# Kernel tuning notes

Hardware: AMD Instinct MI355X
Metric: run time of the kernel (lower is better)

## Reference

```python
import jax, jax.numpy as jnp
import numpy as np

# module hyperparameters (from init_kwargs)
R_MIN, R_MAX = 0.01, 0.6
RH, RW = 64, 64          # retinal_H, retinal_W
H, W = 64, 128           # output pooled H, W
UFR, UFT = 4, 4          # upsampling factors


def make_grid(weight):
    """Vectorized version of get_grid. weight: [B,2].
    Faithful to source: only the top-left [H, W] corner of the
    [H*UFR, W*UFT] grid is written; the rest (torch.empty in the
    original) is set to 0 here for determinism."""
    i = jnp.arange(H, dtype=jnp.float32)
    j = jnp.arange(W, dtype=jnp.float32)
    xg = (i - (H // 2)) / (H / 2.0)
    yg = (j - (W // 2)) / (W / 2.0)
    xx, yy = jnp.meshgrid(xg, yg, indexing="ij")  # [H,W]
    # clamp radius to avoid log(0) = -inf at the center pixel; the resulting
    # coordinate is far out of [-1,1] and gets border-clamped either way.
    logr = jnp.log(jnp.maximum(jnp.sqrt(xx ** 2 + yy ** 2), 1e-12))  # [H,W]
    lo = jnp.log(weight[:, 0] * R_MIN)[:, None, None]  # [B,1,1]
    hi = jnp.log(weight[:, 1] * R_MAX)[:, None, None]  # [B,1,1]
    r = RH * (logr[None] - lo) / (hi - lo)             # [B,H,W]
    a = jnp.arctan2(yy, xx)
    a = jnp.where(a > 0, a, 2.0 * np.pi + a)
    t = 0.5 * a * RW / np.pi                           # [H,W]
    gx = jnp.broadcast_to((t / (RW / 2.0) - 1.0)[None], r.shape)
    gy = r / (RH / 2.0) - 1.0
    small = jnp.stack([gx, gy], axis=-1)               # [B,H,W,2]
    grid = jnp.zeros((weight.shape[0], H * UFR, W * UFT, 2), jnp.float32)
    return grid.at[:, :H, :W, :].set(small)


def grid_sample_border(x, grid):
    """torch.F.grid_sample, mode=bilinear, padding_mode=border, align_corners=False.
    x: [B,C,Hin,Win], grid: [B,Hg,Wg,2] -> [B,C,Hg,Wg]."""
    B, C, Hin, Win = x.shape
    gx, gy = grid[..., 0], grid[..., 1]
    ix = jnp.clip(((gx + 1.0) * Win - 1.0) * 0.5, 0.0, Win - 1.0)
    iy = jnp.clip(((gy + 1.0) * Hin - 1.0) * 0.5, 0.0, Hin - 1.0)
    x0f = jnp.floor(ix)
    y0f = jnp.floor(iy)
    wx = (ix - x0f)[..., None]
    wy = (iy - y0f)[..., None]
    x0 = jnp.clip(x0f.astype(jnp.int32), 0, Win - 1)
    y0 = jnp.clip(y0f.astype(jnp.int32), 0, Hin - 1)
    x1 = jnp.clip(x0 + 1, 0, Win - 1)
    y1 = jnp.clip(y0 + 1, 0, Hin - 1)
    bidx = jnp.arange(B)[:, None, None]
    gather = lambda yi, xi: x[bidx, :, yi, xi]  # [B,Hg,Wg,C]
    out = (gather(y0, x0) * (1 - wx) * (1 - wy)
           + gather(y0, x1) * wx * (1 - wy)
           + gather(y1, x0) * (1 - wx) * wy
           + gather(y1, x1) * wx * wy)
    return jnp.transpose(out, (0, 3, 1, 2))  # [B,C,Hg,Wg]


def setup_inputs() -> dict:
    key = jax.random.key(0)
    k1, k2, k3, k4, k5, k6 = jax.random.split(key, 6)
    B, C, Hin, Win = 8, 64, 224, 224
    Cmid = C // 2  # int(channel * r)
    return {
        "x": jax.random.normal(k1, (B, C, Hin, Win), jnp.float32),
        "l_t_prev": jax.random.uniform(k2, (B, 2), jnp.float32),
        "w1": jax.random.normal(k3, (C, Cmid), jnp.float32) * 0.1,
        "b1": jnp.zeros((Cmid,), jnp.float32),
        "w2": jax.random.normal(k4, (Cmid, 2), jnp.float32) * 0.1,
        "b2": jnp.zeros((2,), jnp.float32),
    }


def reference(x, l_t_prev, w1, b1, w2, b2):
    # att: global avg pool -> fc -> sigmoid
    branch = x.mean(axis=(2, 3))                              # [B,C]
    weight = jax.nn.sigmoid(jax.nn.relu(branch @ w1 + b1) @ w2 + b2)  # [B,2]
    grid = make_grid(weight) + l_t_prev[:, None, None, :]     # [B,Hg,Wg,2]
    sampled = grid_sample_border(x, grid)                     # [B,C,Hg,Wg]
    B, C = sampled.shape[:2]
    pooled = sampled.reshape(B, C, H, UFR, W, UFT).mean(axis=(3, 5))  # AvgPool2d([UFR,UFT])
    return pooled, weight
```

## Files before the change

kernel.cpp:

```cpp
#include <hip/hip_runtime.h>
#include <math.h>

#define B 8
#define C 64
#define HIN 224
#define WIN 224
#define PLANE (HIN*WIN)
#define PLANE4 (PLANE/4)
#define QUART (PLANE4/4)
#define OH 64
#define OW 128
#define OUT_PER_BC (OH*OW)
#define NGRID (OH*OW)
#define POOLED_SIZE (B*C*OH*OW)

#define WS_PARTIAL 0
#define WS_WEIGHT 2048
#define WS_COORDS 4096

#define PI_F 3.14159265358979323846f

__global__ __launch_bounds__(256) void k1_gap(const float* __restrict__ x,
                                              float* __restrict__ ws) {
    int blk = blockIdx.x;
    int bc  = blk >> 2, q = blk & 3;
    const float4* p = (const float4*)x + (size_t)bc * PLANE4 + q * QUART;
    int tid = threadIdx.x;
    float s = 0.f;
#pragma unroll
    for (int k = 0; k < 12; ++k) {
        float4 v = p[tid + k * 256];
        s += (v.x + v.y) + (v.z + v.w);
    }
    if (tid < QUART - 12 * 256) {
        float4 v = p[tid + 12 * 256];
        s += (v.x + v.y) + (v.z + v.w);
    }
    for (int off = 32; off; off >>= 1) s += __shfl_down(s, off, 64);
    __shared__ float lds[4];
    if ((tid & 63) == 0) lds[tid >> 6] = s;
    __syncthreads();
    if (tid == 0) ws[WS_PARTIAL + blk] = lds[0] + lds[1] + lds[2] + lds[3];
}

__global__ __launch_bounds__(256) void k2_mlp(const float* __restrict__ w1,
                                              const float* __restrict__ b1,
                                              const float* __restrict__ w2,
                                              const float* __restrict__ b2,
                                              float* __restrict__ ws,
                                              float* __restrict__ out_weight) {
    __shared__ float branch[B * C];
    __shared__ float hidden[B * 32];
    int tid = threadIdx.x;
    for (int i = tid; i < B * C; i += 256) {
        const float* pp = ws + WS_PARTIAL + i * 4;
        branch[i] = (pp[0] + pp[1] + pp[2] + pp[3]) * (1.0f / PLANE);
    }
    __syncthreads();
    {
        int b = tid >> 5, m = tid & 31;
        float h = b1[m];
        for (int c = 0; c < C; ++c) h += branch[b * C + c] * w1[c * 32 + m];
        hidden[b * 32 + m] = h > 0.f ? h : 0.f;
    }
    __syncthreads();
    if (tid < 16) {
        int bb = tid >> 1, k = tid & 1;
        float s = b2[k];
        for (int mm = 0; mm < 32; ++mm) s += hidden[bb * 32 + mm] * w2[mm * 2 + k];
        float wv = 1.f / (1.f + expf(-s));
        ws[WS_WEIGHT + tid] = wv;
        out_weight[tid] = wv;
    }
}

__global__ __launch_bounds__(256) void k2b_coords(const float* __restrict__ wgt,
                                                  const float* __restrict__ l_t,
                                                  float2* __restrict__ coords) {
    int p = blockIdx.x * 256 + threadIdx.x;
    int b = p >> 13;
    int rem = p & 8191;
    int i = rem >> 7;
    int j = rem & 127;
    float w0 = wgt[b * 2 + 0];
    float w1v = wgt[b * 2 + 1];
    float lo = logf(w0 * 0.01f);
    float hi = logf(w1v * 0.6f);
    float xg = (float)(i - 32) * (1.f / 32.f);
    float yg = (float)(j - 64) * (1.f / 64.f);
    float rr = sqrtf(xg * xg + yg * yg);
    float logr = logf(fmaxf(rr, 1e-12f));
    float r = 64.f * (logr - lo) / (hi - lo);
    float a = atan2f(yg, xg);
    if (!(a > 0.f)) a = 2.f * PI_F + a;
    float t = 0.5f * a * 64.f / PI_F;
    float gx = t * (1.f / 32.f) - 1.f + l_t[b * 2 + 0];
    float gy = r * (1.f / 32.f) - 1.f + l_t[b * 2 + 1];
    float ix = ((gx + 1.f) * (float)WIN - 1.f) * 0.5f;
    float iy = ((gy + 1.f) * (float)HIN - 1.f) * 0.5f;
    ix = fminf(fmaxf(ix, 0.f), (float)(WIN - 1));
    iy = fminf(fmaxf(iy, 0.f), (float)(HIN - 1));
    coords[p] = make_float2(ix, iy);
}

__device__ __forceinline__ float bilinear(const float* __restrict__ p,
                                          float ix, float iy) {
    float x0f = floorf(ix), y0f = floorf(iy);
    int x0 = (int)x0f, y0 = (int)y0f;
    float wx = ix - x0f, wy = iy - y0f;
    int x1 = min(x0 + 1, WIN - 1);
    int y1 = min(y0 + 1, HIN - 1);
    const float* r0 = p + y0 * WIN;
    const float* r1 = p + y1 * WIN;
    float v00 = r0[x0], v01 = r0[x1], v10 = r1[x0], v11 = r1[x1];
    float v0 = v00 + (v01 - v00) * wx;
    float v1 = v10 + (v11 - v10) * wx;
    return v0 + (v1 - v0) * wy;
}

__global__ __launch_bounds__(256) void k3_sample(const float* __restrict__ x,
                                                 const float* __restrict__ l_t,
                                                 const float2* __restrict__ coords,
                                                 float* __restrict__ out) {
    int bc = blockIdx.x;
    int b = bc >> 6;
    int tid = threadIdx.x;
    const float* plane = x + (size_t)bc * PLANE;
    float* o = out + (size_t)bc * OUT_PER_BC;

    float gx = l_t[b * 2 + 0], gy = l_t[b * 2 + 1];
    float ixc = fminf(fmaxf(((gx + 1.f) * (float)WIN - 1.f) * 0.5f, 0.f), (float)(WIN - 1));
    float iyc = fminf(fmaxf(((gy + 1.f) * (float)HIN - 1.f) * 0.5f, 0.f), (float)(HIN - 1));
    float vconst = bilinear(plane, ixc, iyc);

#pragma unroll
    for (int k = 0; k < 32; ++k) {
        int oi = tid + k * 256;
        int h = oi >> 7, w = oi & 127;
        if (!(h < 16 && w < 32)) o[oi] = vconst;
    }

    const float2* cb = coords + b * NGRID;
#pragma unroll
    for (int rr = 0; rr < 2; ++rr) {
        int oi = tid + rr * 256;
        int h = oi >> 5, w = oi & 31;
        float acc = 0.f;
#pragma unroll
        for (int di = 0; di < 4; ++di) {
            const float2* cr = cb + (4 * h + di) * 128 + 4 * w;
#pragma unroll
            for (int dj = 0; dj < 4; ++dj) {
                float2 cxy = cr[dj];
                acc += bilinear(plane, cxy.x, cxy.y);
            }
        }
        o[h * 128 + w] = acc * (1.f / 16.f);
    }
}

extern "C" void kernel_launch(void* const* d_in, const int* in_sizes, int n_in,
                              void* d_out, int out_size, void* d_ws, size_t ws_size,
                              hipStream_t stream) {
    const float* x   = (const float*)d_in[0];
    const float* l_t = (const float*)d_in[1];
    const float* w1  = (const float*)d_in[2];
    const float* b1  = (const float*)d_in[3];
    const float* w2  = (const float*)d_in[4];
    const float* b2  = (const float*)d_in[5];
    float* out = (float*)d_out;
    float* ws  = (float*)d_ws;

    k1_gap<<<dim3(B * C * 4), dim3(256), 0, stream>>>(x, ws);
    k2_mlp<<<dim3(1), dim3(256), 0, stream>>>(w1, b1, w2, b2, ws, out + POOLED_SIZE);
    k2b_coords<<<dim3(NGRID * B / 256), dim3(256), 0, stream>>>(ws + WS_WEIGHT, l_t,
                                                                (float2*)(ws + WS_COORDS));
    k3_sample<<<dim3(B * C), dim3(256), 0, stream>>>(x, l_t,
                                                     (const float2*)(ws + WS_COORDS), out);
}
```

Baseline: 175.5 us.

## Fuse constant fill into GAP kernel, merge MLP with coords, split corner sampling

Moves the constant-value output fill (everything outside the 16x32 corner) into the global-average-pool kernel with float4 stores, so it overlaps with the pooling reads. The single-block MLP is folded into the coordinate kernel, where each block recomputes its batch's MLP, removing one launch and a serial one-block stage. The corner sampling is spread over four times as many blocks, with pairs of threads splitting the 4x4 taps and combining them via a shuffle, to raise parallelism. The costs are redundant MLP work in every coordinate block and extra gather traffic in the fill kernel.

Result: no change. 176.8 us (+0.8%).

```diff
diff --git a/kernel.cpp b/kernel.cpp
--- a/kernel.cpp
+++ b/kernel.cpp
@@ -15,93 +15,9 @@
 #define POOLED_SIZE (B*C*OH*OW)
 
 #define WS_PARTIAL 0
-#define WS_WEIGHT 2048
 #define WS_COORDS 4096
 
 #define PI_F 3.14159265358979323846f
-
-__global__ __launch_bounds__(256) void k1_gap(const float* __restrict__ x,
-                                              float* __restrict__ ws) {
-    int blk = blockIdx.x;
-    int bc  = blk >> 2, q = blk & 3;
-    const float4* p = (const float4*)x + (size_t)bc * PLANE4 + q * QUART;
-    int tid = threadIdx.x;
-    float s = 0.f;
-#pragma unroll
-    for (int k = 0; k < 12; ++k) {
-        float4 v = p[tid + k * 256];
-        s += (v.x + v.y) + (v.z + v.w);
-    }
-    if (tid < QUART - 12 * 256) {
-        float4 v = p[tid + 12 * 256];
-        s += (v.x + v.y) + (v.z + v.w);
-    }
-    for (int off = 32; off; off >>= 1) s += __shfl_down(s, off, 64);
-    __shared__ float lds[4];
-    if ((tid & 63) == 0) lds[tid >> 6] = s;
-    __syncthreads();
-    if (tid == 0) ws[WS_PARTIAL + blk] = lds[0] + lds[1] + lds[2] + lds[3];
-}
-
-__global__ __launch_bounds__(256) void k2_mlp(const float* __restrict__ w1,
-                                              const float* __restrict__ b1,
-                                              const float* __restrict__ w2,
-                                              const float* __restrict__ b2,
-                                              float* __restrict__ ws,
-                                              float* __restrict__ out_weight) {
-    __shared__ float branch[B * C];
-    __shared__ float hidden[B * 32];
-    int tid = threadIdx.x;
-    for (int i = tid; i < B * C; i += 256) {
-        const float* pp = ws + WS_PARTIAL + i * 4;
-        branch[i] = (pp[0] + pp[1] + pp[2] + pp[3]) * (1.0f / PLANE);
-    }
-    __syncthreads();
-    {
-        int b = tid >> 5, m = tid & 31;
-        float h = b1[m];
-        for (int c = 0; c < C; ++c) h += branch[b * C + c] * w1[c * 32 + m];
-        hidden[b * 32 + m] = h > 0.f ? h : 0.f;
-    }
-    __syncthreads();
-    if (tid < 16) {
-        int bb = tid >> 1, k = tid & 1;
-        float s = b2[k];
-        for (int mm = 0; mm < 32; ++mm) s += hidden[bb * 32 + mm] * w2[mm * 2 + k];
-        float wv = 1.f / (1.f + expf(-s));
-        ws[WS_WEIGHT + tid] = wv;
-        out_weight[tid] = wv;
-    }
-}
-
-__global__ __launch_bounds__(256) void k2b_coords(const float* __restrict__ wgt,
-                                                  const float* __restrict__ l_t,
-                                                  float2* __restrict__ coords) {
-    int p = blockIdx.x * 256 + threadIdx.x;
-    int b = p >> 13;
-    int rem = p & 8191;
-    int i = rem >> 7;
-    int j = rem & 127;
-    float w0 = wgt[b * 2 + 0];
-    float w1v = wgt[b * 2 + 1];
-    float lo = logf(w0 * 0.01f);
-    float hi = logf(w1v * 0.6f);
-    float xg = (float)(i - 32) * (1.f / 32.f);
-    float yg = (float)(j - 64) * (1.f / 64.f);
-    float rr = sqrtf(xg * xg + yg * yg);
-    float logr = logf(fmaxf(rr, 1e-12f));
-    float r = 64.f * (logr - lo) / (hi - lo);
-    float a = atan2f(yg, xg);
-    if (!(a > 0.f)) a = 2.f * PI_F + a;
-    float t = 0.5f * a * 64.f / PI_F;
-    float gx = t * (1.f / 32.f) - 1.f + l_t[b * 2 + 0];
-    float gy = r * (1.f / 32.f) - 1.f + l_t[b * 2 + 1];
-    float ix = ((gx + 1.f) * (float)WIN - 1.f) * 0.5f;
-    float iy = ((gy + 1.f) * (float)HIN - 1.f) * 0.5f;
-    ix = fminf(fmaxf(ix, 0.f), (float)(WIN - 1));
-    iy = fminf(fmaxf(iy, 0.f), (float)(HIN - 1));
-    coords[p] = make_float2(ix, iy);
-}
 
 __device__ __forceinline__ float bilinear(const float* __restrict__ p,
                                           float ix, float iy) {
@@ -118,45 +34,148 @@
     return v0 + (v1 - v0) * wy;
 }
 
-__global__ __launch_bounds__(256) void k3_sample(const float* __restrict__ x,
-                                                 const float* __restrict__ l_t,
-                                                 const float2* __restrict__ coords,
-                                                 float* __restrict__ out) {
-    int bc = blockIdx.x;
-    int b = bc >> 6;
+__global__ __launch_bounds__(256) void k1_gap_fill(const float* __restrict__ x,
+                                                   const float* __restrict__ l_t,
+                                                   float* __restrict__ ws,
+                                                   float* __restrict__ out) {
+    int blk = blockIdx.x;
+    int bc  = blk >> 2, q = blk & 3;
+    int b   = bc >> 6;
     int tid = threadIdx.x;
+
+    const float4* p = (const float4*)x + (size_t)bc * PLANE4 + q * QUART;
+    float s = 0.f;
+#pragma unroll
+    for (int k = 0; k < 12; ++k) {
+        float4 v = p[tid + k * 256];
+        s += (v.x + v.y) + (v.z + v.w);
+    }
+    if (tid < QUART - 12 * 256) {
+        float4 v = p[tid + 12 * 256];
+        s += (v.x + v.y) + (v.z + v.w);
+    }
+
     const float* plane = x + (size_t)bc * PLANE;
-    float* o = out + (size_t)bc * OUT_PER_BC;
-
     float gx = l_t[b * 2 + 0], gy = l_t[b * 2 + 1];
     float ixc = fminf(fmaxf(((gx + 1.f) * (float)WIN - 1.f) * 0.5f, 0.f), (float)(WIN - 1));
     float iyc = fminf(fmaxf(((gy + 1.f) * (float)HIN - 1.f) * 0.5f, 0.f), (float)(HIN - 1));
-    float vconst = bilinear(plane, ixc, iyc);
+    float vc = bilinear(plane, ixc, iyc);
+    float4 vc4 = make_float4(vc, vc, vc, vc);
 
+    float4* o4 = (float4*)(out + (size_t)bc * OUT_PER_BC);
+    if (q == 0) {
 #pragma unroll
-    for (int k = 0; k < 32; ++k) {
-        int oi = tid + k * 256;
-        int h = oi >> 7, w = oi & 127;
-        if (!(h < 16 && w < 32)) o[oi] = vconst;
+        for (int k = 0; k < 2; ++k) {
+            int f4i = tid + k * 256;
+            if (f4i < 384) {
+                int row = f4i / 24;
+                int c4  = f4i - row * 24 + 8;
+                o4[row * 32 + c4] = vc4;
+            }
+        }
+    } else {
+        o4[q * 512 + tid]       = vc4;
+        o4[q * 512 + 256 + tid] = vc4;
     }
 
-    const float2* cb = coords + b * NGRID;
+    for (int off = 32; off; off >>= 1) s += __shfl_down(s, off, 64);
+    __shared__ float lds[4];
+    if ((tid & 63) == 0) lds[tid >> 6] = s;
+    __syncthreads();
+    if (tid == 0) ws[WS_PARTIAL + blk] = lds[0] + lds[1] + lds[2] + lds[3];
+}
+
+__global__ __launch_bounds__(256) void k2_coords(const float* __restrict__ w1,
+                                                 const float* __restrict__ b1,
+                                                 const float* __restrict__ w2,
+                                                 const float* __restrict__ b2,
+                                                 const float* __restrict__ l_t,
+                                                 const float* __restrict__ ws,
+                                                 float* __restrict__ out_weight,
+                                                 float2* __restrict__ coords) {
+    int tid = threadIdx.x;
+    int blk = blockIdx.x;
+    int b   = blk >> 5;
+
+    __shared__ float branch[C];
+    __shared__ float hidden[32];
+    __shared__ float wpair[2];
+
+    if (tid < C) {
+        const float* pp = ws + WS_PARTIAL + (b * C + tid) * 4;
+        branch[tid] = (pp[0] + pp[1] + pp[2] + pp[3]) * (1.0f / PLANE);
+    }
+    __syncthreads();
+    if (tid < 32) {
+        float h = b1[tid];
+        for (int c = 0; c < C; ++c) h += branch[c] * w1[c * 32 + tid];
+        hidden[tid] = h > 0.f ? h : 0.f;
+    }
+    __syncthreads();
+    if (tid < 2) {
+        float sacc = b2[tid];
+        for (int m = 0; m < 32; ++m) sacc += hidden[m] * w2[m * 2 + tid];
+        float wv = 1.f / (1.f + expf(-sacc));
+        wpair[tid] = wv;
+        if ((blk & 31) == 0) out_weight[b * 2 + tid] = wv;
+    }
+    __syncthreads();
+
+    float w0  = wpair[0];
+    float w1v = wpair[1];
+    float lo = logf(w0 * 0.01f);
+    float hi = logf(w1v * 0.6f);
+
+    int p   = blk * 256 + tid;
+    int rem = p & 8191;
+    int i = rem >> 7;
+    int j = rem & 127;
+    float xg = (float)(i - 32) * (1.f / 32.f);
+    float yg = (float)(j - 64) * (1.f / 64.f);
+    float rr = sqrtf(xg * xg + yg * yg);
+    float logr = logf(fmaxf(rr, 1e-12f));
+    float r = 64.f * (logr - lo) / (hi - lo);
+    float a = atan2f(yg, xg);
+    if (!(a > 0.f)) a = 2.f * PI_F + a;
+    float t = 0.5f * a * 64.f / PI_F;
+    float gxv = t * (1.f / 32.f) - 1.f + l_t[b * 2 + 0];
+    float gyv = r * (1.f / 32.f) - 1.f + l_t[b * 2 + 1];
+    float ix = ((gxv + 1.f) * (float)WIN - 1.f) * 0.5f;
+    float iy = ((gyv + 1.f) * (float)HIN - 1.f) * 0.5f;
+    ix = fminf(fmaxf(ix, 0.f), (float)(WIN - 1));
+    iy = fminf(fmaxf(iy, 0.f), (float)(HIN - 1));
+    coords[p] = make_float2(ix, iy);
+}
+
+__global__ __launch_bounds__(256) void k3_corner(const float* __restrict__ x,
+                                                 const float2* __restrict__ coords,
+                                                 float* __restrict__ out) {
+    int blk = blockIdx.x;
+    int bc  = blk >> 2, q = blk & 3;
+    int b   = bc >> 6;
+    int tid = threadIdx.x;
+
+    int out_local = tid >> 1;
+    int half      = tid & 1;
+    int h = q * 4 + (out_local >> 5);
+    int w = out_local & 31;
+
+    const float*  plane = x + (size_t)bc * PLANE;
+    const float2* cb    = coords + b * NGRID;
+
+    float acc = 0.f;
 #pragma unroll
-    for (int rr = 0; rr < 2; ++rr) {
-        int oi = tid + rr * 256;
-        int h = oi >> 5, w = oi & 31;
-        float acc = 0.f;
+    for (int fi2 = 0; fi2 < 2; ++fi2) {
+        int fi = 4 * h + 2 * half + fi2;
+        const float2* cr = cb + fi * 128 + 4 * w;
 #pragma unroll
-        for (int di = 0; di < 4; ++di) {
-            const float2* cr = cb + (4 * h + di) * 128 + 4 * w;
-#pragma unroll
-            for (int dj = 0; dj < 4; ++dj) {
-                float2 cxy = cr[dj];
-                acc += bilinear(plane, cxy.x, cxy.y);
-            }
+        for (int dj = 0; dj < 4; ++dj) {
+            float2 cxy = cr[dj];
+            acc += bilinear(plane, cxy.x, cxy.y);
         }
-        o[h * 128 + w] = acc * (1.f / 16.f);
     }
+    acc += __shfl_xor(acc, 1, 64);
+    if (half == 0) out[(size_t)bc * OUT_PER_BC + h * 128 + w] = acc * (1.f / 16.f);
 }
 
 extern "C" void kernel_launch(void* const* d_in, const int* in_sizes, int n_in,
@@ -171,10 +190,9 @@
     float* out = (float*)d_out;
     float* ws  = (float*)d_ws;
 
-    k1_gap<<<dim3(B * C * 4), dim3(256), 0, stream>>>(x, ws);
-    k2_mlp<<<dim3(1), dim3(256), 0, stream>>>(w1, b1, w2, b2, ws, out + POOLED_SIZE);
-    k2b_coords<<<dim3(NGRID * B / 256), dim3(256), 0, stream>>>(ws + WS_WEIGHT, l_t,
-                                                                (float2*)(ws + WS_COORDS));
-    k3_sample<<<dim3(B * C), dim3(256), 0, stream>>>(x, l_t,
-                                                     (const float2*)(ws + WS_COORDS), out);
+    k1_gap_fill<<<dim3(B * C * 4), dim3(256), 0, stream>>>(x, l_t, ws, out);
+    k2_coords<<<dim3(NGRID * B / 256), dim3(256), 0, stream>>>(
+        w1, b1, w2, b2, l_t, ws, out + POOLED_SIZE, (float2*)(ws + WS_COORDS));
+    k3_corner<<<dim3(B * C * 4), dim3(256), 0, stream>>>(
+        x, (const float2*)(ws + WS_COORDS), out);
 }
```
